# Kernel tuning notes

Measured on AMD Instinct MI355X. Metric: run time of the kernel, lower is better.

## Reference

```python
import jax, jax.numpy as jnp
import numpy as np

N_NODES = 50000


def _gcn_conv(x, W, b, src, dst, norm, n_nodes):
    # x: [N, Fin], W: [Fin, Fout]
    h = x @ W                                   # [N, Fout]
    msg = h[src] * norm[:, None]                # [E+N, Fout] edge messages
    out = jax.ops.segment_sum(msg, dst, num_segments=n_nodes)
    return out + b


def reference(x, edge_index, W1, b1, W2, b2):
    n = x.shape[0]
    # add self-loops (PyG GCNConv default add_self_loops=True)
    loop = jnp.arange(n, dtype=edge_index.dtype)
    src = jnp.concatenate([edge_index[0], loop])
    dst = jnp.concatenate([edge_index[1], loop])
    # symmetric degree normalization: deg over destination with unit weights
    deg = jax.ops.segment_sum(jnp.ones_like(dst, dtype=x.dtype), dst, num_segments=n)
    dinv = jnp.where(deg > 0, jax.lax.rsqrt(deg), 0.0)
    norm = dinv[src] * dinv[dst]                # [E+N]
    h = _gcn_conv(x, W1, b1, src, dst, norm, n)
    h = jax.nn.relu(h)
    out = _gcn_conv(h, W2, b2, src, dst, norm, n)
    return out


def setup_inputs() -> dict:
    key = jax.random.key(0)
    k1, k2, k3, k4 = jax.random.split(key, 4)
    n, e, fin, hid, fout = N_NODES, 800000, 128, 128, 64
    x = jax.random.normal(k1, (n, fin), dtype=jnp.float32)
    edge_index = jax.random.randint(k2, (2, e), 0, n, dtype=jnp.int64)
    # Glorot-ish init for linear weights, zero bias (PyG default)
    W1 = jax.random.normal(k3, (fin, hid), dtype=jnp.float32) / np.sqrt(fin)
    b1 = jnp.zeros((hid,), dtype=jnp.float32)
    W2 = jax.random.normal(k4, (hid, fout), dtype=jnp.float32) / np.sqrt(hid)
    b2 = jnp.zeros((fout,), dtype=jnp.float32)
    return {"x": x, "edge_index": edge_index, "W1": W1, "b1": b1, "W2": W2, "b2": b2}
```

## Files before the change

### kernel.cpp

```cpp
#include <hip/hip_runtime.h>
#include <hip/hip_bf16.h>


constexpr int FIN = 128;
constexpr int HID = 128;
constexpr int FOUT = 64;
constexpr int CAP = 48;
constexpr int NPB = 98;
constexpr int BCAP = 3072;
constexpr int OVF_MAX = 65536;

typedef __attribute__((ext_vector_type(8))) short s16x8;
typedef __attribute__((ext_vector_type(4))) float f32x4;
typedef __attribute__((ext_vector_type(2))) float f32x2;

static __device__ __forceinline__ float bf2f(__hip_bfloat16 v) { return __bfloat162float(v); }
static __device__ __forceinline__ float lo2f(unsigned u) { union { unsigned i; float f; } c; c.i = u << 16; return c.f; }
static __device__ __forceinline__ float hi2f(unsigned u) { union { unsigned i; float f; } c; c.i = u & 0xffff0000u; return c.f; }
static __device__ __forceinline__ unsigned short f2bfu(float f) {
    __hip_bfloat16 h = __float2bfloat16(f);
    union { __hip_bfloat16 h; unsigned short u; } c; c.h = h; return c.u;
}
static __device__ __forceinline__ unsigned pack2(float a, float b) {
    return (unsigned)f2bfu(a) | ((unsigned)f2bfu(b) << 16);
}
static __device__ __forceinline__ f32x2 unpk(unsigned u) {
    union { unsigned i; float f; } a, b;
    a.i = u << 16; b.i = u & 0xffff0000u;
    f32x2 r; r[0] = a.f; r[1] = b.f; return r;
}
static __device__ __forceinline__ void acc_add(f32x2* acc, uint4 v) {
    acc[0] += unpk(v.x); acc[1] += unpk(v.y);
    acc[2] += unpk(v.z); acc[3] += unpk(v.w);
}
static __device__ __forceinline__ void acc_fma(f32x2* acc, uint4 v, float w) {
    f32x2 ws; ws[0] = w; ws[1] = w;
    acc[0] += ws * unpk(v.x); acc[1] += ws * unpk(v.y);
    acc[2] += ws * unpk(v.z); acc[3] += ws * unpk(v.w);
}

struct SW { int s; float w; };

__global__ __launch_bounds__(256) void k_detect(const unsigned* __restrict__ xw,
                                                const int* __restrict__ eiw,
                                                int E, int* __restrict__ flags,
                                                int* __restrict__ gcur,
                                                int* __restrict__ cnt, int N, int zero_cnt) {
    if (zero_cnt)
        for (long i = (long)blockIdx.x * 256 + threadIdx.x; i < N; i += (long)gridDim.x * 256)
            cnt[i] = 0;
    if (blockIdx.x != 0) return;
    for (int i = threadIdx.x; i < 514; i += 256) gcur[i] = 0;
    __shared__ int s_bf16like, s_oddnz;
    if (threadIdx.x == 0) { s_bf16like = 0; s_oddnz = 0; }
    __syncthreads();
    int c = 0;
    for (int i = threadIdx.x; i < 4096; i += 256) {
        unsigned ex = ((xw[i] & 0xffffu) >> 7) & 0xffu;
        if (ex >= 117u && ex <= 130u) c++;
    }
    atomicAdd(&s_bf16like, c);
    int nz = 0;
    for (int i = threadIdx.x; i < 2048; i += 256)
        if (eiw[2 * i + 1] != 0) nz++;
    atomicAdd(&s_oddnz, nz);
    __syncthreads();
    if (threadIdx.x == 0) {
        flags[0] = (s_bf16like < 2048) ? 1 : 0;
        flags[1] = (s_oddnz == 0) ? 1 : 0;
    }
}

__global__ __launch_bounds__(256) void k_mega(const void* __restrict__ Xp,
                                              const void* __restrict__ Wp,
                                              const int* __restrict__ ei, int E, int N,
                                              int nbuk, int GB,
                                              int* __restrict__ gcur,
                                              unsigned* __restrict__ pairs,
                                              int2* __restrict__ ovfA,
                                              int* __restrict__ ovfAcnt,
                                              __hip_bfloat16* __restrict__ G,
                                              const int* __restrict__ flags) {
    extern __shared__ __align__(16) char smem[];
    const int tid = threadIdx.x;
    if ((int)blockIdx.x < GB) {
        short* Wt = (short*)smem;
        const bool f32m = flags[0] != 0;
        for (int i = tid; i < 128 * 128; i += 256) {
            int k = i >> 7, n = i & 127;
            float wv = f32m ? ((const float*)Wp)[(long)k * 128 + n]
                            : bf2f(((const __hip_bfloat16*)Wp)[(long)k * 128 + n]);
            Wt[n * 136 + k] = (short)f2bfu(wv);
        }
        __syncthreads();
        const int w = tid >> 6, lane = tid & 63;
        const int m = lane & 15, quad = lane >> 4;
        const int rowA = blockIdx.x * 64 + w * 16 + m;
        const int rowc = rowA < N ? rowA : N - 1;
        s16x8 afr[4];
#pragma unroll
        for (int kc = 0; kc < 4; ++kc) {
            const int k0 = kc * 32 + quad * 8;
            if (!f32m) {
                afr[kc] = *(const s16x8*)((const __hip_bfloat16*)Xp + (long)rowc * 128 + k0);
            } else {
                const float* p = (const float*)Xp + (long)rowc * 128 + k0;
                s16x8 t;
#pragma unroll
                for (int j = 0; j < 8; ++j) t[j] = (short)f2bfu(p[j]);
                afr[kc] = t;
            }
        }
        const int rbase = blockIdx.x * 64 + w * 16 + quad * 4;
#pragma unroll
        for (int ct = 0; ct < 8; ++ct) {
            f32x4 acc = {0.f, 0.f, 0.f, 0.f};
#pragma unroll
            for (int kc = 0; kc < 4; ++kc) {
                s16x8 bfr = *(const s16x8*)&Wt[(ct * 16 + m) * 136 + kc * 32 + quad * 8];
                acc = __builtin_amdgcn_mfma_f32_16x16x32_bf16(afr[kc], bfr, acc, 0, 0, 0);
            }
            const int plane = ct >> 2;
            const int cp = (ct & 3) * 16 + m;
#pragma unroll
            for (int r = 0; r < 4; ++r) {
                int rr = rbase + r;
                if (rr < N)
                    G[(long)plane * N * 64 + (long)rr * 64 + cp] = __float2bfloat16(acc[r]);
            }
        }
    } else {
        int* hist = (int*)smem;
        int* gbase = hist + 512;
        const long base = (long)(blockIdx.x - GB) * 2048;
        const bool i64 = flags[1] != 0;
        int se[8], de[8];
        for (int b = tid; b < nbuk; b += 256) hist[b] = 0;
        __syncthreads();
#pragma unroll
        for (int j = 0; j < 8; ++j) {
            long i = base + j * 256 + tid;
            int s = 0, d = -1;
            if (i < E) {
                if (i64) { s = ((const int2*)ei)[i].x; d = ((const int2*)(ei + 2 * (long)E))[i].x; }
                else     { s = ei[i]; d = ei[(long)E + i]; }
                if ((unsigned)s >= (unsigned)N || (unsigned)d >= (unsigned)N) d = -1;
            }
            se[j] = s; de[j] = d;
            if (d >= 0) atomicAdd(&hist[d / NPB], 1);
        }
        __syncthreads();
        for (int b = tid; b < nbuk; b += 256) {
            int h = hist[b];
            gbase[b] = h > 0 ? atomicAdd(&gcur[b], h) : 0;
            hist[b] = 0;
        }
        __syncthreads();
#pragma unroll
        for (int j = 0; j < 8; ++j) {
            int d = de[j];
            if (d < 0) continue;
            int b = d / NPB;
            int p = gbase[b] + atomicAdd(&hist[b], 1);
            if (p < BCAP) {
                pairs[(long)b * BCAP + p] = ((unsigned)(d - b * NPB) << 16) | (unsigned)se[j];
            } else {
                int op = atomicAdd(ovfAcnt, 1);
                if (op < OVF_MAX) ovfA[op] = make_int2(d, se[j]);
            }
        }
    }
}

__global__ __launch_bounds__(256) void k_binB(const int* __restrict__ gcur,
                                              const unsigned* __restrict__ pairs,
                                              const int2* __restrict__ ovfA,
                                              const int* __restrict__ ovfAcnt,
                                              int* __restrict__ cnt,
                                              float* __restrict__ dinv,
                                              unsigned short* __restrict__ slots,
                                              int2* __restrict__ ovf2,
                                              int* __restrict__ ovf2cnt, int N) {
    __shared__ int cntL[NPB];
    __shared__ __align__(16) unsigned short slotsL[NPB * CAP];
    const int b = blockIdx.x;
    const int tid = threadIdx.x;
    const int d0 = b * NPB;
    const int nd = min(NPB, N - d0);
    if (nd <= 0) return;
    for (int i = tid; i < NPB; i += 256) cntL[i] = 0;
    __syncthreads();
    const int c = min(gcur[b], BCAP);
    const unsigned* pb = pairs + (long)b * BCAP;
    for (int i = tid; i < c; i += 256) {
        unsigned p = pb[i];
        int ld = p >> 16;
        int pos = atomicAdd(&cntL[ld], 1);
        if (pos < CAP) {
            slotsL[ld * CAP + pos] = (unsigned short)(p & 0xffffu);
        } else {
            int op = atomicAdd(ovf2cnt, 1);
            if (op < OVF_MAX) ovf2[op] = make_int2(d0 + ld, (int)(p & 0xffffu));
        }
    }
    int na = *ovfAcnt; na = na < OVF_MAX ? na : OVF_MAX;
    for (int i = tid; i < na; i += 256) {
        int2 p = ovfA[i];
        int ld = p.x - d0;
        if ((unsigned)ld < (unsigned)nd) {
            int pos = atomicAdd(&cntL[ld], 1);
            if (pos < CAP) {
                slotsL[ld * CAP + pos] = (unsigned short)p.y;
            } else {
                int op = atomicAdd(ovf2cnt, 1);
                if (op < OVF_MAX) ovf2[op] = p;
            }
        }
    }
    __syncthreads();
    for (int ld = tid; ld < nd; ld += 256) {
        const int mloc = min(cntL[ld], CAP);
        unsigned short* row = &slotsL[ld * CAP];
        for (int a = 1; a < mloc; ++a) {
            const unsigned short key = row[a];
            int p = a - 1;
            while (p >= 0 && row[p] > key) { row[p + 1] = row[p]; --p; }
            row[p + 1] = key;
        }
    }
    __syncthreads();
    for (int i = tid; i < nd; i += 256) {
        cnt[d0 + i] = cntL[i];
        dinv[d0 + i] = rsqrtf((float)(cntL[i] + 1));
    }
    const uint4* sv = (const uint4*)slotsL;
    uint4* gv = (uint4*)(slots + (long)d0 * CAP);
    const int total8 = (nd * CAP) >> 3;
    for (int i = tid; i < total8; i += 256) gv[i] = sv[i];
}

__global__ __launch_bounds__(256) void k_build_direct(const int* __restrict__ ei, int E, int N,
                                                      int* __restrict__ cnt,
                                                      int* __restrict__ slots,
                                                      int2* __restrict__ ovf2,
                                                      int* __restrict__ ovf2cnt,
                                                      const int* __restrict__ flags) {
    long i = (long)blockIdx.x * 256 + threadIdx.x;
    if (i >= E) return;
    int s, d;
    if (flags[1]) { s = ((const int2*)ei)[i].x; d = ((const int2*)(ei + 2 * (long)E))[i].x; }
    else          { s = ei[i]; d = ei[(long)E + i]; }
    if ((unsigned)s >= (unsigned)N || (unsigned)d >= (unsigned)N) return;
    int pos = atomicAdd(&cnt[d], 1);
    if (pos < CAP) {
        slots[(long)d * CAP + pos] = s;
    } else {
        int op = atomicAdd(ovf2cnt, 1);
        if (op < OVF_MAX) ovf2[op] = make_int2(d, s);
    }
}

template<int CT, int SPLIT>
__global__ __launch_bounds__(256) void k_gemm(const void* __restrict__ Xp, int x_follows_flag,
                                              const void* __restrict__ Wp,
                                              const int* __restrict__ cnt,
                                              __hip_bfloat16* __restrict__ G,
                                              const int* __restrict__ flags, int N) {
    constexpr int C = CT * 16;
    __shared__ __align__(16) short Wt[C * 136];
    const bool f32m = flags[0] != 0;
    const bool xf32 = (x_follows_flag != 0) && f32m;
    const int tid = threadIdx.x;
    for (int i = tid; i < 128 * C; i += 256) {
        int k = i / C, n = i % C;
        float wv = f32m ? ((const float*)Wp)[(long)k * C + n]
                        : bf2f(((const __hip_bfloat16*)Wp)[(long)k * C + n]);
        Wt[n * 136 + k] = (short)f2bfu(wv);
    }
    __syncthreads();
    const int w = tid >> 6, lane = tid & 63;
    const int m = lane & 15, quad = lane >> 4;
    const int rowA = blockIdx.x * 64 + w * 16 + m;
    const int rowc = rowA < N ? rowA : N - 1;
    s16x8 afr[4];
#pragma unroll
    for (int kc = 0; kc < 4; ++kc) {
        const int k0 = kc * 32 + quad * 8;
        if (!xf32) {
            afr[kc] = *(const s16x8*)((const __hip_bfloat16*)Xp + (long)rowc * 128 + k0);
        } else {
            const float* p = (const float*)Xp + (long)rowc * 128 + k0;
            s16x8 t;
#pragma unroll
            for (int j = 0; j < 8; ++j) t[j] = (short)f2bfu(p[j]);
            afr[kc] = t;
        }
    }
    const int rbase = blockIdx.x * 64 + w * 16 + quad * 4;
    float dv[4];
#pragma unroll
    for (int r = 0; r < 4; ++r) {
        int rr = min(rbase + r, N - 1);
        dv[r] = rsqrtf((float)(cnt[rr] + 1));
    }
#pragma unroll
    for (int ct = 0; ct < CT; ++ct) {
        f32x4 acc = {0.f, 0.f, 0.f, 0.f};
#pragma unroll
        for (int kc = 0; kc < 4; ++kc) {
            s16x8 bfr = *(const s16x8*)&Wt[(ct * 16 + m) * 136 + kc * 32 + quad * 8];
            acc = __builtin_amdgcn_mfma_f32_16x16x32_bf16(afr[kc], bfr, acc, 0, 0, 0);
        }
#pragma unroll
        for (int r = 0; r < 4; ++r) {
            int rr = rbase + r;
            if (rr < N) {
                long off;
                if (SPLIT) {
                    const int plane = ct / (CT / 2);
                    const int cp = (ct % (CT / 2)) * 16 + m;
                    off = (long)plane * N * (C / 2) + (long)rr * (C / 2) + cp;
                } else {
                    off = (long)rr * C + ct * 16 + m;
                }
                G[off] = __float2bfloat16(dv[r] * acc[r]);
            }
        }
    }
}

__global__ __launch_bounds__(256) void k_gather1b(const __hip_bfloat16* __restrict__ G,
                                                  const int* __restrict__ cnt,
                                                  const float* __restrict__ dinv,
                                                  const unsigned short* __restrict__ slots,
                                                  const int2* __restrict__ ovf2,
                                                  const int* __restrict__ ovf2cnt,
                                                  const void* __restrict__ b1,
                                                  __hip_bfloat16* __restrict__ h1,
                                                  const int* __restrict__ flags, int N) {
    __shared__ int cntL[32];
    __shared__ float wsL[32];
    __shared__ __align__(16) SW swL[32 * 49];
    const int tid = threadIdx.x;
    const int n0 = blockIdx.x * 32;
    const int nd = min(32, N - n0);
    for (int i = tid; i < nd; i += 256) {
        cntL[i] = cnt[n0 + i];
        wsL[i] = dinv[n0 + i];
    }
    __syncthreads();
    for (int j = tid; j < 32 * CAP; j += 256) {
        const int ni = j / CAP, sl = j - ni * CAP;
        if (ni < nd) {
            const int mm = min(cntL[ni], CAP);
            if (sl < mm) {
                const int s = slots[(long)(n0 + ni) * CAP + sl];
                swL[ni * 49 + sl].s = s;
                swL[ni * 49 + sl].w = dinv[s];
            }
        }
    }
    __syncthreads();
    const int grp = tid >> 3, lane = tid & 7;
    if (grp >= nd) return;
    const int node = n0 + grp;
    const int cd = cntL[grp];
    const int m = cd < CAP ? cd : CAP;
    const float wself = wsL[grp];
    const SW* sw = &swL[grp * 49];
    const bool f32m = flags[0] != 0;
    for (int P = 0; P < 2; ++P) {
        const __hip_bfloat16* Gp = G + (long)P * N * 64;
        f32x2 acc2[4] = {};
        float* acc = (float*)acc2;
        acc_fma(acc2, ((const uint4*)(Gp + (long)node * 64))[lane], wself);
        int i = 0;
        for (; i + 7 < m; i += 8) {
            SW a0 = sw[i], a1 = sw[i + 1], a2 = sw[i + 2], a3 = sw[i + 3];
            SW a4 = sw[i + 4], a5 = sw[i + 5], a6 = sw[i + 6], a7 = sw[i + 7];
            uint4 v0 = ((const uint4*)(Gp + (long)a0.s * 64))[lane];
            uint4 v1 = ((const uint4*)(Gp + (long)a1.s * 64))[lane];
            uint4 v2 = ((const uint4*)(Gp + (long)a2.s * 64))[lane];
            uint4 v3 = ((const uint4*)(Gp + (long)a3.s * 64))[lane];
            uint4 v4 = ((const uint4*)(Gp + (long)a4.s * 64))[lane];
            uint4 v5 = ((const uint4*)(Gp + (long)a5.s * 64))[lane];
            uint4 v6 = ((const uint4*)(Gp + (long)a6.s * 64))[lane];
            uint4 v7 = ((const uint4*)(Gp + (long)a7.s * 64))[lane];
            acc_fma(acc2, v0, a0.w); acc_fma(acc2, v1, a1.w);
            acc_fma(acc2, v2, a2.w); acc_fma(acc2, v3, a3.w);
            acc_fma(acc2, v4, a4.w); acc_fma(acc2, v5, a5.w);
            acc_fma(acc2, v6, a6.w); acc_fma(acc2, v7, a7.w);
        }
        for (; i + 3 < m; i += 4) {
            SW a0 = sw[i], a1 = sw[i + 1], a2 = sw[i + 2], a3 = sw[i + 3];
            uint4 v0 = ((const uint4*)(Gp + (long)a0.s * 64))[lane];
            uint4 v1 = ((const uint4*)(Gp + (long)a1.s * 64))[lane];
            uint4 v2 = ((const uint4*)(Gp + (long)a2.s * 64))[lane];
            uint4 v3 = ((const uint4*)(Gp + (long)a3.s * 64))[lane];
            acc_fma(acc2, v0, a0.w); acc_fma(acc2, v1, a1.w);
            acc_fma(acc2, v2, a2.w); acc_fma(acc2, v3, a3.w);
        }
        for (; i < m; ++i) {
            SW a = sw[i];
            acc_fma(acc2, ((const uint4*)(Gp + (long)a.s * 64))[lane], a.w);
        }
        if (cd > CAP) {
            int oc = *ovf2cnt; oc = oc < OVF_MAX ? oc : OVF_MAX;
            for (int j = 0; j < oc; ++j)
                if (ovf2[j].x == node) {
                    int s0 = ovf2[j].y;
                    acc_fma(acc2, ((const uint4*)(Gp + (long)s0 * 64))[lane], dinv[s0]);
                }
        }
        const int c0 = P * 64 + lane * 8;
        float bv[8];
        if (f32m) {
            const float4* bp = (const float4*)((const float*)b1 + c0);
            float4 b0 = bp[0], b1v = bp[1];
            bv[0] = b0.x; bv[1] = b0.y; bv[2] = b0.z; bv[3] = b0.w;
            bv[4] = b1v.x; bv[5] = b1v.y; bv[6] = b1v.z; bv[7] = b1v.w;
        } else {
            uint4 b = *(const uint4*)((const __hip_bfloat16*)b1 + c0);
            bv[0] = lo2f(b.x); bv[1] = hi2f(b.x); bv[2] = lo2f(b.y); bv[3] = hi2f(b.y);
            bv[4] = lo2f(b.z); bv[5] = hi2f(b.z); bv[6] = lo2f(b.w); bv[7] = hi2f(b.w);
        }
        float o[8];
#pragma unroll
        for (int c = 0; c < 8; ++c) {
            float v = wself * acc[c] + bv[c];
            o[c] = v > 0.f ? v : 0.f;
        }
        uint4 pv = { pack2(o[0], o[1]), pack2(o[2], o[3]), pack2(o[4], o[5]), pack2(o[6], o[7]) };
        ((uint4*)(h1 + (long)node * 128 + P * 64))[lane] = pv;
    }
}

template<int F, int LAYER1, typename ST>
__global__ __launch_bounds__(256) void k_gather(const __hip_bfloat16* __restrict__ G,
                                                const int* __restrict__ cnt,
                                                const ST* __restrict__ slots,
                                                const int2* __restrict__ ovf2,
                                                const int* __restrict__ ovf2cnt,
                                                const void* __restrict__ bias,
                                                void* __restrict__ outp,
                                                const int* __restrict__ flags, int N) {
    constexpr int L = F / 8;
    constexpr int NODES = 256 / L;
    const int tid = threadIdx.x;
    const int grp = tid / L, lane = tid % L;
    const int node = blockIdx.x * NODES + grp;
    if (node >= N) return;
    const int cd = cnt[node];
    const float wself = rsqrtf((float)(cd + 1));
    const int m = cd < CAP ? cd : CAP;
    const ST* sl = slots + (long)node * CAP;
    f32x2 acc2[4] = {};
    float* acc = (float*)acc2;
    acc_add(acc2, ((const uint4*)(G + (long)node * F))[lane]);
    int i = 0;
    for (; i + 7 < m; i += 8) {
        int s0 = sl[i], s1 = sl[i + 1], s2 = sl[i + 2], s3 = sl[i + 3];
        int s4 = sl[i + 4], s5 = sl[i + 5], s6 = sl[i + 6], s7 = sl[i + 7];
        uint4 v0 = ((const uint4*)(G + (long)s0 * F))[lane];
        uint4 v1 = ((const uint4*)(G + (long)s1 * F))[lane];
        uint4 v2 = ((const uint4*)(G + (long)s2 * F))[lane];
        uint4 v3 = ((const uint4*)(G + (long)s3 * F))[lane];
        uint4 v4 = ((const uint4*)(G + (long)s4 * F))[lane];
        uint4 v5 = ((const uint4*)(G + (long)s5 * F))[lane];
        uint4 v6 = ((const uint4*)(G + (long)s6 * F))[lane];
        uint4 v7 = ((const uint4*)(G + (long)s7 * F))[lane];
        acc_add(acc2, v0); acc_add(acc2, v1); acc_add(acc2, v2); acc_add(acc2, v3);
        acc_add(acc2, v4); acc_add(acc2, v5); acc_add(acc2, v6); acc_add(acc2, v7);
    }
    for (; i + 3 < m; i += 4) {
        int s0 = sl[i], s1 = sl[i + 1], s2 = sl[i + 2], s3 = sl[i + 3];
        uint4 v0 = ((const uint4*)(G + (long)s0 * F))[lane];
        uint4 v1 = ((const uint4*)(G + (long)s1 * F))[lane];
        uint4 v2 = ((const uint4*)(G + (long)s2 * F))[lane];
        uint4 v3 = ((const uint4*)(G + (long)s3 * F))[lane];
        acc_add(acc2, v0); acc_add(acc2, v1); acc_add(acc2, v2); acc_add(acc2, v3);
    }
    for (; i < m; ++i)
        acc_add(acc2, ((const uint4*)(G + (long)sl[i] * F))[lane]);
    if (cd > CAP) {
        int oc = *ovf2cnt; oc = oc < OVF_MAX ? oc : OVF_MAX;
        for (int j = 0; j < oc; ++j)
            if (ovf2[j].x == node)
                acc_add(acc2, ((const uint4*)(G + (long)ovf2[j].y * F))[lane]);
    }
    const bool f32m = flags[0] != 0;
    const int c0 = lane * 8;
    float bv[8];
    if (f32m) {
        const float4* bp = (const float4*)((const float*)bias + c0);
        float4 b0 = bp[0], b1 = bp[1];
        bv[0] = b0.x; bv[1] = b0.y; bv[2] = b0.z; bv[3] = b0.w;
        bv[4] = b1.x; bv[5] = b1.y; bv[6] = b1.z; bv[7] = b1.w;
    } else {
        uint4 b = *(const uint4*)((const __hip_bfloat16*)bias + c0);
        bv[0] = lo2f(b.x); bv[1] = hi2f(b.x); bv[2] = lo2f(b.y); bv[3] = hi2f(b.y);
        bv[4] = lo2f(b.z); bv[5] = hi2f(b.z); bv[6] = lo2f(b.w); bv[7] = hi2f(b.w);
    }
    float o[8];
#pragma unroll
    for (int c = 0; c < 8; ++c) {
        float v = wself * acc[c] + bv[c];
        o[c] = (LAYER1 && v < 0.f) ? 0.f : v;
    }
    if (LAYER1 || !f32m) {
        uint4 pv = { pack2(o[0], o[1]), pack2(o[2], o[3]), pack2(o[4], o[5]), pack2(o[6], o[7]) };
        ((uint4*)outp)[(long)node * L + lane] = pv;
    } else {
        float4* op = (float4*)((float*)outp + (long)node * F + c0);
        op[0] = make_float4(o[0], o[1], o[2], o[3]);
        op[1] = make_float4(o[4], o[5], o[6], o[7]);
    }
}

extern "C" void kernel_launch(void* const* d_in, const int* in_sizes, int n_in,
                              void* d_out, int out_size, void* d_ws, size_t ws_size,
                              hipStream_t stream) {
    const void* x  = d_in[0];
    const int*  ei = (const int*)d_in[1];
    const void* W1 = d_in[2];
    const void* b1 = d_in[3];
    const void* W2 = d_in[4];
    const void* b2 = d_in[5];

    const int N = in_sizes[0] / FIN;
    const int E = in_sizes[1] / 2;
    const int nbuk = (N + NPB - 1) / NPB;

    char* ws = (char*)d_ws;
    int*   flags   = (int*)ws;
    int*   gcur    = (int*)(ws + 4096);
    int*   ovfAcnt = gcur + 512;
    int*   ovf2cnt = gcur + 513;
    int*   cnt     = (int*)(ws + 65536);
    float* dinv    = (float*)(ws + 266240);
    int2*  ovfA    = (int2*)(ws + 524288);
    int2*  ovf2    = (int2*)(ws + 1048576);
    unsigned short* slots16 = (unsigned short*)(ws + 2097152);
    int*   slots32 = (int*)(ws + 2097152);
    __hip_bfloat16* g  = (__hip_bfloat16*)(ws + 11730944);
    __hip_bfloat16* g2 = g;
    unsigned* pairs = (unsigned*)(ws + 24530944);
    __hip_bfloat16* h1 = (__hip_bfloat16*)(ws + 24530944);

    const int GB = (N + 63) / 64;
    const int AB = (E + 2047) / 2048;
    const int EB = (E + 255) / 256;

    if (N <= 65536 && nbuk <= 512) {
        k_detect<<<1, 256, 0, stream>>>((const unsigned*)x, ei, E, flags, gcur, cnt, N, 0);
        k_mega<<<GB + AB, 256, 34816, stream>>>(x, W1, ei, E, N, nbuk, GB,
                                                gcur, pairs, ovfA, ovfAcnt, g, flags);
        k_binB<<<nbuk, 256, 0, stream>>>(gcur, pairs, ovfA, ovfAcnt, cnt, dinv, slots16, ovf2, ovf2cnt, N);
        const int GBL = (N + 31) / 32;
        k_gather1b<<<GBL, 256, 0, stream>>>(g, cnt, dinv, slots16, ovf2, ovf2cnt, b1, h1, flags, N);
        k_gemm<4, 0><<<GB, 256, 0, stream>>>(h1, 0, W2, cnt, g2, flags, N);
        k_gather<64, 0, unsigned short><<<(N + 31) / 32, 256, 0, stream>>>(
            g2, cnt, slots16, ovf2, ovf2cnt, b2, d_out, flags, N);
    } else {
        k_detect<<<64, 256, 0, stream>>>((const unsigned*)x, ei, E, flags, gcur, cnt, N, 1);
        k_build_direct<<<EB, 256, 0, stream>>>(ei, E, N, cnt, slots32, ovf2, ovf2cnt, flags);
        k_gemm<8, 0><<<GB, 256, 0, stream>>>(x, 1, W1, cnt, g, flags, N);
        k_gather<128, 1, int><<<(N + 15) / 16, 256, 0, stream>>>(
            g, cnt, slots32, ovf2, ovf2cnt, b1, h1, flags, N);
        k_gemm<4, 0><<<GB, 256, 0, stream>>>(h1, 0, W2, cnt, g2, flags, N);
        k_gather<64, 0, int><<<(N + 31) / 32, 256, 0, stream>>>(
            g2, cnt, slots32, ovf2, ovf2cnt, b2, d_out, flags, N);
    }
}
```

Before: 232.6 us.

## Store layer-1 features row-major and gather both halves in one pass

```diff
diff --git a/kernel.cpp b/kernel.cpp
--- a/kernel.cpp
+++ b/kernel.cpp
@@ -120,13 +120,12 @@
                 s16x8 bfr = *(const s16x8*)&Wt[(ct * 16 + m) * 136 + kc * 32 + quad * 8];
                 acc = __builtin_amdgcn_mfma_f32_16x16x32_bf16(afr[kc], bfr, acc, 0, 0, 0);
             }
-            const int plane = ct >> 2;
-            const int cp = (ct & 3) * 16 + m;
+            const int cp = ct * 16 + m;
 #pragma unroll
             for (int r = 0; r < 4; ++r) {
                 int rr = rbase + r;
                 if (rr < N)
-                    G[(long)plane * N * 64 + (long)rr * 64 + cp] = __float2bfloat16(acc[r]);
+                    G[(long)rr * 128 + cp] = __float2bfloat16(acc[r]);
             }
         }
     } else {
@@ -215,17 +214,6 @@
                 int op = atomicAdd(ovf2cnt, 1);
                 if (op < OVF_MAX) ovf2[op] = p;
             }
-        }
-    }
-    __syncthreads();
-    for (int ld = tid; ld < nd; ld += 256) {
-        const int mloc = min(cntL[ld], CAP);
-        unsigned short* row = &slotsL[ld * CAP];
-        for (int a = 1; a < mloc; ++a) {
-            const unsigned short key = row[a];
-            int p = a - 1;
-            while (p >= 0 && row[p] > key) { row[p + 1] = row[p]; --p; }
-            row[p + 1] = key;
         }
     }
     __syncthreads();
@@ -329,7 +317,7 @@
     }
 }
 
-__global__ __launch_bounds__(256) void k_gather1b(const __hip_bfloat16* __restrict__ G,
+__global__ __launch_bounds__(256) void k_gather1c(const __hip_bfloat16* __restrict__ G,
                                                   const int* __restrict__ cnt,
                                                   const float* __restrict__ dinv,
                                                   const unsigned short* __restrict__ slots,
@@ -369,70 +357,78 @@
     const float wself = wsL[grp];
     const SW* sw = &swL[grp * 49];
     const bool f32m = flags[0] != 0;
-    for (int P = 0; P < 2; ++P) {
-        const __hip_bfloat16* Gp = G + (long)P * N * 64;
-        f32x2 acc2[4] = {};
-        float* acc = (float*)acc2;
-        acc_fma(acc2, ((const uint4*)(Gp + (long)node * 64))[lane], wself);
-        int i = 0;
-        for (; i + 7 < m; i += 8) {
-            SW a0 = sw[i], a1 = sw[i + 1], a2 = sw[i + 2], a3 = sw[i + 3];
-            SW a4 = sw[i + 4], a5 = sw[i + 5], a6 = sw[i + 6], a7 = sw[i + 7];
-            uint4 v0 = ((const uint4*)(Gp + (long)a0.s * 64))[lane];
-            uint4 v1 = ((const uint4*)(Gp + (long)a1.s * 64))[lane];
-            uint4 v2 = ((const uint4*)(Gp + (long)a2.s * 64))[lane];
-            uint4 v3 = ((const uint4*)(Gp + (long)a3.s * 64))[lane];
-            uint4 v4 = ((const uint4*)(Gp + (long)a4.s * 64))[lane];
-            uint4 v5 = ((const uint4*)(Gp + (long)a5.s * 64))[lane];
-            uint4 v6 = ((const uint4*)(Gp + (long)a6.s * 64))[lane];
-            uint4 v7 = ((const uint4*)(Gp + (long)a7.s * 64))[lane];
-            acc_fma(acc2, v0, a0.w); acc_fma(acc2, v1, a1.w);
-            acc_fma(acc2, v2, a2.w); acc_fma(acc2, v3, a3.w);
-            acc_fma(acc2, v4, a4.w); acc_fma(acc2, v5, a5.w);
-            acc_fma(acc2, v6, a6.w); acc_fma(acc2, v7, a7.w);
-        }
-        for (; i + 3 < m; i += 4) {
-            SW a0 = sw[i], a1 = sw[i + 1], a2 = sw[i + 2], a3 = sw[i + 3];
-            uint4 v0 = ((const uint4*)(Gp + (long)a0.s * 64))[lane];
-            uint4 v1 = ((const uint4*)(Gp + (long)a1.s * 64))[lane];
-            uint4 v2 = ((const uint4*)(Gp + (long)a2.s * 64))[lane];
-            uint4 v3 = ((const uint4*)(Gp + (long)a3.s * 64))[lane];
-            acc_fma(acc2, v0, a0.w); acc_fma(acc2, v1, a1.w);
-            acc_fma(acc2, v2, a2.w); acc_fma(acc2, v3, a3.w);
-        }
-        for (; i < m; ++i) {
-            SW a = sw[i];
-            acc_fma(acc2, ((const uint4*)(Gp + (long)a.s * 64))[lane], a.w);
-        }
-        if (cd > CAP) {
-            int oc = *ovf2cnt; oc = oc < OVF_MAX ? oc : OVF_MAX;
-            for (int j = 0; j < oc; ++j)
-                if (ovf2[j].x == node) {
-                    int s0 = ovf2[j].y;
-                    acc_fma(acc2, ((const uint4*)(Gp + (long)s0 * 64))[lane], dinv[s0]);
-                }
-        }
-        const int c0 = P * 64 + lane * 8;
-        float bv[8];
-        if (f32m) {
-            const float4* bp = (const float4*)((const float*)b1 + c0);
-            float4 b0 = bp[0], b1v = bp[1];
-            bv[0] = b0.x; bv[1] = b0.y; bv[2] = b0.z; bv[3] = b0.w;
-            bv[4] = b1v.x; bv[5] = b1v.y; bv[6] = b1v.z; bv[7] = b1v.w;
-        } else {
-            uint4 b = *(const uint4*)((const __hip_bfloat16*)b1 + c0);
-            bv[0] = lo2f(b.x); bv[1] = hi2f(b.x); bv[2] = lo2f(b.y); bv[3] = hi2f(b.y);
-            bv[4] = lo2f(b.z); bv[5] = hi2f(b.z); bv[6] = lo2f(b.w); bv[7] = hi2f(b.w);
-        }
-        float o[8];
-#pragma unroll
-        for (int c = 0; c < 8; ++c) {
-            float v = wself * acc[c] + bv[c];
-            o[c] = v > 0.f ? v : 0.f;
-        }
-        uint4 pv = { pack2(o[0], o[1]), pack2(o[2], o[3]), pack2(o[4], o[5]), pack2(o[6], o[7]) };
-        ((uint4*)(h1 + (long)node * 128 + P * 64))[lane] = pv;
-    }
+    f32x2 accA[4] = {};
+    f32x2 accB[4] = {};
+    float* aA = (float*)accA;
+    float* aB = (float*)accB;
+    {
+        const uint4* sp = (const uint4*)(G + (long)node * 128);
+        acc_fma(accA, sp[lane], wself);
+        acc_fma(accB, sp[8 + lane], wself);
+    }
+    int i = 0;
+    for (; i + 3 < m; i += 4) {
+        SW a0 = sw[i], a1 = sw[i + 1], a2 = sw[i + 2], a3 = sw[i + 3];
+        const uint4* p0 = (const uint4*)(G + (long)a0.s * 128);
+        const uint4* p1 = (const uint4*)(G + (long)a1.s * 128);
+        const uint4* p2 = (const uint4*)(G + (long)a2.s * 128);
+        const uint4* p3 = (const uint4*)(G + (long)a3.s * 128);
+        uint4 v0a = p0[lane], v0b = p0[8 + lane];
+        uint4 v1a = p1[lane], v1b = p1[8 + lane];
+        uint4 v2a = p2[lane], v2b = p2[8 + lane];
+        uint4 v3a = p3[lane], v3b = p3[8 + lane];
+        acc_fma(accA, v0a, a0.w); acc_fma(accB, v0b, a0.w);
+        acc_fma(accA, v1a, a1.w); acc_fma(accB, v1b, a1.w);
+        acc_fma(accA, v2a, a2.w); acc_fma(accB, v2b, a2.w);
+        acc_fma(accA, v3a, a3.w); acc_fma(accB, v3b, a3.w);
+    }
+    for (; i < m; ++i) {
+        SW a = sw[i];
+        const uint4* p = (const uint4*)(G + (long)a.s * 128);
+        acc_fma(accA, p[lane], a.w);
+        acc_fma(accB, p[8 + lane], a.w);
+    }
+    if (cd > CAP) {
+        int oc = *ovf2cnt; oc = oc < OVF_MAX ? oc : OVF_MAX;
+        for (int j = 0; j < oc; ++j)
+            if (ovf2[j].x == node) {
+                int s0 = ovf2[j].y;
+                float w0 = dinv[s0];
+                const uint4* p = (const uint4*)(G + (long)s0 * 128);
+                acc_fma(accA, p[lane], w0);
+                acc_fma(accB, p[8 + lane], w0);
+            }
+    }
+    float bvA[8], bvB[8];
+    if (f32m) {
+        const float4* bpA = (const float4*)((const float*)b1 + lane * 8);
+        const float4* bpB = (const float4*)((const float*)b1 + 64 + lane * 8);
+        float4 a0 = bpA[0], a1 = bpA[1], b0 = bpB[0], b1v = bpB[1];
+        bvA[0] = a0.x; bvA[1] = a0.y; bvA[2] = a0.z; bvA[3] = a0.w;
+        bvA[4] = a1.x; bvA[5] = a1.y; bvA[6] = a1.z; bvA[7] = a1.w;
+        bvB[0] = b0.x; bvB[1] = b0.y; bvB[2] = b0.z; bvB[3] = b0.w;
+        bvB[4] = b1v.x; bvB[5] = b1v.y; bvB[6] = b1v.z; bvB[7] = b1v.w;
+    } else {
+        uint4 ba = *(const uint4*)((const __hip_bfloat16*)b1 + lane * 8);
+        uint4 bb = *(const uint4*)((const __hip_bfloat16*)b1 + 64 + lane * 8);
+        bvA[0] = lo2f(ba.x); bvA[1] = hi2f(ba.x); bvA[2] = lo2f(ba.y); bvA[3] = hi2f(ba.y);
+        bvA[4] = lo2f(ba.z); bvA[5] = hi2f(ba.z); bvA[6] = lo2f(ba.w); bvA[7] = hi2f(ba.w);
+        bvB[0] = lo2f(bb.x); bvB[1] = hi2f(bb.x); bvB[2] = lo2f(bb.y); bvB[3] = hi2f(bb.y);
+        bvB[4] = lo2f(bb.z); bvB[5] = hi2f(bb.z); bvB[6] = lo2f(bb.w); bvB[7] = hi2f(bb.w);
+    }
+    float oA[8], oB[8];
+#pragma unroll
+    for (int c = 0; c < 8; ++c) {
+        float vA = wself * aA[c] + bvA[c];
+        float vB = wself * aB[c] + bvB[c];
+        oA[c] = vA > 0.f ? vA : 0.f;
+        oB[c] = vB > 0.f ? vB : 0.f;
+    }
+    uint4 pA = { pack2(oA[0], oA[1]), pack2(oA[2], oA[3]), pack2(oA[4], oA[5]), pack2(oA[6], oA[7]) };
+    uint4 pB = { pack2(oB[0], oB[1]), pack2(oB[2], oB[3]), pack2(oB[4], oB[5]), pack2(oB[6], oB[7]) };
+    uint4* hp = (uint4*)(h1 + (long)node * 128);
+    hp[lane] = pA;
+    hp[8 + lane] = pB;
 }
 
 template<int F, int LAYER1, typename ST>
@@ -557,7 +553,7 @@
                                                 gcur, pairs, ovfA, ovfAcnt, g, flags);
         k_binB<<<nbuk, 256, 0, stream>>>(gcur, pairs, ovfA, ovfAcnt, cnt, dinv, slots16, ovf2, ovf2cnt, N);
         const int GBL = (N + 31) / 32;
-        k_gather1b<<<GBL, 256, 0, stream>>>(g, cnt, dinv, slots16, ovf2, ovf2cnt, b1, h1, flags, N);
+        k_gather1c<<<GBL, 256, 0, stream>>>(g, cnt, dinv, slots16, ovf2, ovf2cnt, b1, h1, flags, N);
         k_gemm<4, 0><<<GB, 256, 0, stream>>>(h1, 0, W2, cnt, g2, flags, N);
         k_gather<64, 0, unsigned short><<<(N + 31) / 32, 256, 0, stream>>>(
             g2, cnt, slots16, ovf2, ovf2cnt, b2, d_out, flags, N);
```

Result: faster. 192.7 us (-17.2%).
